# Kernel optimization log

Measured on AMD Instinct MI355X. Metric: run time of the kernel, lower is better.

Reference implementation:

```python
import jax, jax.numpy as jnp
import numpy as np

LORA_ALPHA = 2.0

def setup_inputs() -> dict:
    key = jax.random.key(0)
    k1, k2, k3, k4 = jax.random.split(key, 4)
    B, S, D_IN, D_OUT, R = 4, 2048, 4096, 4096, 16
    x = jax.random.normal(k1, (B, S, D_IN), dtype=jnp.float32)
    weight = jax.random.normal(k2, (D_OUT, D_IN), dtype=jnp.float32) * (1.0 / np.sqrt(D_IN))
    lora_A = jax.random.normal(k3, (R, D_IN), dtype=jnp.float32) * (1.0 / np.sqrt(D_IN))
    lora_B = jax.random.normal(k4, (D_OUT, R), dtype=jnp.float32) * 0.02
    return {"x": x, "weight": weight, "lora_A": lora_A, "lora_B": lora_B}

def reference(x, weight, lora_A, lora_B):
    # main_out = F.linear(x, weight) = x @ weight.T
    main_out = jnp.einsum('bsd,od->bso', x, weight)
    # Faithful to source: materialize lora_weight = B @ A (out x in), then full linear
    lora_weight = lora_B @ lora_A  # [out, in]
    lora_out = jnp.einsum('bsd,od->bso', x, lora_weight) * LORA_ALPHA
    return main_out + lora_out
```

## Files before the change

kernel.cpp:

```cpp
#include <hip/hip_runtime.h>
#include <stdint.h>

typedef __attribute__((ext_vector_type(8))) short bf16x8;
typedef __attribute__((ext_vector_type(4))) float f32x4;

#define GM 8192
#define GN 4096
#define GK 4096
#define KTILES (GK / 64)

__device__ __forceinline__ unsigned short f2bf(float f) {
  union { float f; unsigned int u; } c; c.f = f;
  unsigned int u = c.u;
  unsigned int r = u + 0x7FFFu + ((u >> 16) & 1u);
  return (unsigned short)(r >> 16);
}

__global__ __launch_bounds__(256) void cvt_x_kernel(const float* __restrict__ x,
                                                    unsigned short* __restrict__ xb) {
  int i = blockIdx.x * 256 + threadIdx.x;
  const float4* p = (const float4*)x + (size_t)i * 2;
  float4 a = p[0], b = p[1];
  unsigned short t[8] = { f2bf(a.x), f2bf(a.y), f2bf(a.z), f2bf(a.w),
                          f2bf(b.x), f2bf(b.y), f2bf(b.z), f2bf(b.w) };
  int4 pk; __builtin_memcpy(&pk, t, 16);
  ((int4*)xb)[i] = pk;
}

__global__ __launch_bounds__(256) void weff_kernel(const float* __restrict__ w,
                                                   const float* __restrict__ lA,
                                                   const float* __restrict__ lB,
                                                   unsigned short* __restrict__ wb) {
  const int K = GK;
  int idx = blockIdx.x * 256 + threadIdx.x;
  int cg = idx & 511;
  int rg = idx >> 9;
  int i0 = cg << 3;
  int o0 = rg << 3;

  float acc[8][8];
#pragma unroll
  for (int r = 0; r < 8; ++r)
#pragma unroll
    for (int c = 0; c < 8; ++c) acc[r][c] = 0.f;

#pragma unroll
  for (int r = 0; r < 16; ++r) {
    float4 a0 = *(const float4*)(lA + (size_t)r * K + i0);
    float4 a1 = *(const float4*)(lA + (size_t)r * K + i0 + 4);
    float av[8] = { a0.x, a0.y, a0.z, a0.w, a1.x, a1.y, a1.z, a1.w };
#pragma unroll
    for (int row = 0; row < 8; ++row) {
      float b = lB[(size_t)(o0 + row) * 16 + r];
#pragma unroll
      for (int c = 0; c < 8; ++c) acc[row][c] += b * av[c];
    }
  }

#pragma unroll
  for (int row = 0; row < 8; ++row) {
    float4 w0 = *(const float4*)(w + (size_t)(o0 + row) * K + i0);
    float4 w1 = *(const float4*)(w + (size_t)(o0 + row) * K + i0 + 4);
    unsigned short t[8] = {
      f2bf(w0.x + 2.0f * acc[row][0]), f2bf(w0.y + 2.0f * acc[row][1]),
      f2bf(w0.z + 2.0f * acc[row][2]), f2bf(w0.w + 2.0f * acc[row][3]),
      f2bf(w1.x + 2.0f * acc[row][4]), f2bf(w1.y + 2.0f * acc[row][5]),
      f2bf(w1.z + 2.0f * acc[row][6]), f2bf(w1.w + 2.0f * acc[row][7]) };
    int4 pk; __builtin_memcpy(&pk, t, 16);
    *(int4*)(wb + (size_t)(o0 + row) * K + i0) = pk;
  }
}


__device__ __forceinline__ void gload16(const unsigned short* g, char* l) {
  __builtin_amdgcn_global_load_lds((__attribute__((address_space(1))) void*)g,
                                   (__attribute__((address_space(3))) void*)l, 16, 0, 0);
}

__device__ __forceinline__ void bar() {
  asm volatile("" ::: "memory");
  __builtin_amdgcn_s_barrier();
  asm volatile("" ::: "memory");
}

#define MFMA_BF16(a, b, c) __builtin_amdgcn_mfma_f32_16x16x32_bf16((a), (b), (c), 0, 0, 0)

template <int HALF>
__device__ __forceinline__ void stage_half(const unsigned short* A, const unsigned short* B,
                                           char* smem, int bm0, int bn0, int w, int lane,
                                           int kt, int buf) {
  int sr, isB;
  if constexpr (HALF == 0)      { sr = w + (w & 4);                   isB = 0; }
  else if constexpr (HALF == 1) { sr = ((w >> 1) << 2) + (w & 1);     isB = 1; }
  else if constexpr (HALF == 2) { sr = ((w >> 1) << 2) + (w & 1) + 2; isB = 1; }
  else                          { sr = w + (w & 4) + 4;               isB = 0; }
  const unsigned short* mat = isB ? B : A;
  const int grow = (isB ? bn0 : bm0) + sr * 16 + (lane >> 2);
  const int gcol = ((lane & 3) * 8) ^ ((lane & 32) ? 16 : 0);
#pragma unroll
  for (int sc = 0; sc < 2; ++sc) {
    const unsigned short* src = mat + (size_t)grow * GK + kt * 64 + sc * 32 + gcol;
    char* dst = smem + (buf << 16) + (isB ? 32768 : 0) + ((sr * 2 + sc) << 10);
    gload16(src, dst);
  }
}

__device__ __forceinline__ bf16x8 ldsA(const char* smem, int buf, int sr, int sc, int foff) {
  return *(const bf16x8*)(smem + (buf << 16) + ((sr * 2 + sc) << 10) + foff);
}
__device__ __forceinline__ bf16x8 ldsB(const char* smem, int buf, int sr, int sc, int foff) {
  return *(const bf16x8*)(smem + (buf << 16) + 32768 + ((sr * 2 + sc) << 10) + foff);
}

__global__ __launch_bounds__(512, 2) void gemm_bt_kernel(const unsigned short* __restrict__ A,
                                                         const unsigned short* __restrict__ B,
                                                         float* __restrict__ C) {
  __shared__ alignas(16) char smem[131072];

  const int t = threadIdx.x, lane = t & 63, w = t >> 6;
  const int wm = w >> 2, wn = w & 3;

  const int bid = blockIdx.x;
  const int wg  = (bid & 7) * (512 / 8) + (bid >> 3);
  const int bx = wg & 15, by = wg >> 4;
  const int bm0 = by * 256, bn0 = bx * 256;

  int foff = (lane & 15) * 64 + ((lane >> 4) << 4);
  foff ^= ((foff >> 9) & 1) << 5;

  stage_half<0>(A, B, smem, bm0, bn0, w, lane, 0, 0);
  stage_half<1>(A, B, smem, bm0, bn0, w, lane, 0, 0);
  stage_half<2>(A, B, smem, bm0, bn0, w, lane, 0, 0);
  stage_half<3>(A, B, smem, bm0, bn0, w, lane, 0, 0);
  stage_half<0>(A, B, smem, bm0, bn0, w, lane, 1, 1);
  asm volatile("s_waitcnt vmcnt(6)" ::: "memory");
  bar();

  f32x4 acc[8][4] = {};
  bf16x8 av[4][2], bv0[2][2], bv1[2][2];

  for (int kt = 0; kt < KTILES; ++kt) {
    const int cur = kt & 1;
    const bool n1 = (kt + 1 < KTILES);
    const bool n2 = (kt + 2 < KTILES);

#pragma unroll
    for (int mi = 0; mi < 4; ++mi) {
      av[mi][0] = ldsA(smem, cur, wm * 8 + mi, 0, foff);
      av[mi][1] = ldsA(smem, cur, wm * 8 + mi, 1, foff);
    }
#pragma unroll
    for (int ni = 0; ni < 2; ++ni) {
      bv0[ni][0] = ldsB(smem, cur, wn * 4 + ni, 0, foff);
      bv0[ni][1] = ldsB(smem, cur, wn * 4 + ni, 1, foff);
    }
    if (n1) {
      stage_half<1>(A, B, smem, bm0, bn0, w, lane, kt + 1, cur ^ 1);
      asm volatile("s_waitcnt vmcnt(6)" ::: "memory");
    } else {
      asm volatile("s_waitcnt vmcnt(2)" ::: "memory");
    }
    bar();
    asm volatile("s_waitcnt lgkmcnt(0)" ::: "memory");
    __builtin_amdgcn_s_setprio(1);
#pragma unroll
    for (int mi = 0; mi < 4; ++mi)
#pragma unroll
      for (int ni = 0; ni < 2; ++ni) {
        acc[mi][ni] = MFMA_BF16(av[mi][0], bv0[ni][0], acc[mi][ni]);
        acc[mi][ni] = MFMA_BF16(av[mi][1], bv0[ni][1], acc[mi][ni]);
      }
    __builtin_amdgcn_s_setprio(0);
    bar();

#pragma unroll
    for (int ni = 0; ni < 2; ++ni) {
      bv1[ni][0] = ldsB(smem, cur, wn * 4 + 2 + ni, 0, foff);
      bv1[ni][1] = ldsB(smem, cur, wn * 4 + 2 + ni, 1, foff);
    }
    if (n1) {
      stage_half<2>(A, B, smem, bm0, bn0, w, lane, kt + 1, cur ^ 1);
      asm volatile("s_waitcnt vmcnt(6)" ::: "memory");
    } else {
      asm volatile("s_waitcnt vmcnt(0)" ::: "memory");
    }
    bar();
    asm volatile("s_waitcnt lgkmcnt(0)" ::: "memory");
    __builtin_amdgcn_s_setprio(1);
#pragma unroll
    for (int mi = 0; mi < 4; ++mi)
#pragma unroll
      for (int ni = 0; ni < 2; ++ni) {
        acc[mi][2 + ni] = MFMA_BF16(av[mi][0], bv1[ni][0], acc[mi][2 + ni]);
        acc[mi][2 + ni] = MFMA_BF16(av[mi][1], bv1[ni][1], acc[mi][2 + ni]);
      }
    __builtin_amdgcn_s_setprio(0);
    bar();

#pragma unroll
    for (int mi = 0; mi < 4; ++mi) {
      av[mi][0] = ldsA(smem, cur, wm * 8 + 4 + mi, 0, foff);
      av[mi][1] = ldsA(smem, cur, wm * 8 + 4 + mi, 1, foff);
    }
    if (n1) stage_half<3>(A, B, smem, bm0, bn0, w, lane, kt + 1, cur ^ 1);
    bar();
    asm volatile("s_waitcnt lgkmcnt(0)" ::: "memory");
    __builtin_amdgcn_s_setprio(1);
#pragma unroll
    for (int mi = 0; mi < 4; ++mi)
#pragma unroll
      for (int ni = 0; ni < 2; ++ni) {
        acc[4 + mi][2 + ni] = MFMA_BF16(av[mi][0], bv1[ni][0], acc[4 + mi][2 + ni]);
        acc[4 + mi][2 + ni] = MFMA_BF16(av[mi][1], bv1[ni][1], acc[4 + mi][2 + ni]);
      }
    __builtin_amdgcn_s_setprio(0);
    bar();

    if (n2) stage_half<0>(A, B, smem, bm0, bn0, w, lane, kt + 2, cur);
    if (n1) {
      if (n2) asm volatile("s_waitcnt vmcnt(6)" ::: "memory");
      else    asm volatile("s_waitcnt vmcnt(4)" ::: "memory");
    }
    bar();
    __builtin_amdgcn_s_setprio(1);
#pragma unroll
    for (int mi = 0; mi < 4; ++mi)
#pragma unroll
      for (int ni = 0; ni < 2; ++ni) {
        acc[4 + mi][ni] = MFMA_BF16(av[mi][0], bv0[ni][0], acc[4 + mi][ni]);
        acc[4 + mi][ni] = MFMA_BF16(av[mi][1], bv0[ni][1], acc[4 + mi][ni]);
      }
    __builtin_amdgcn_s_setprio(0);
    bar();
  }

  const int orow = (lane >> 4) << 2;
#pragma unroll
  for (int mi = 0; mi < 8; ++mi) {
#pragma unroll
    for (int ni = 0; ni < 4; ++ni) {
      float* cp = C + (size_t)(bm0 + wm * 128 + mi * 16 + orow) * GN
                    + (bn0 + wn * 64 + ni * 16 + (lane & 15));
#pragma unroll
      for (int r = 0; r < 4; ++r)
        cp[(size_t)r * GN] = acc[mi][ni][r];
    }
  }
}

extern "C" void kernel_launch(void* const* d_in, const int* in_sizes, int n_in,
                              void* d_out, int out_size, void* d_ws, size_t ws_size,
                              hipStream_t stream) {
  const float* x  = (const float*)d_in[0];
  const float* w  = (const float*)d_in[1];
  const float* lA = (const float*)d_in[2];
  const float* lB = (const float*)d_in[3];
  float* out = (float*)d_out;

  const int M = GM, N = GN, K = GK;

  unsigned short* xb = (unsigned short*)d_ws;
  unsigned short* wb = xb + (size_t)M * K;

  cvt_x_kernel<<<dim3((M * K / 8) / 256), dim3(256), 0, stream>>>(x, xb);
  weff_kernel<<<dim3((N / 8) * (K / 8) / 256), dim3(256), 0, stream>>>(w, lA, lB, wb);
  gemm_bt_kernel<<<dim3((M / 256) * (N / 256)), dim3(512), 0, stream>>>(xb, wb, out);
}
```

Measured before the change: 293.5 us.

## Interleave LDS fragment loads with MFMA and drop per-phase barriers

Restructures the GEMM main loop so each LDS fragment read is issued during the preceding MFMA block instead of before it. Fragments for the next k-tile are prefetched at the end of the current iteration, and the phase-end barriers plus explicit lgkmcnt waits are removed so fewer syncs sit on the critical path. The intent is to hide LDS read latency behind matrix math. The risk is LDS hazards between buffer reuse and global-to-LDS staging once barriers are gone, and higher register pressure.

```diff
diff --git a/kernel.cpp b/kernel.cpp
--- a/kernel.cpp
+++ b/kernel.cpp
@@ -139,99 +139,101 @@
   f32x4 acc[8][4] = {};
   bf16x8 av[4][2], bv0[2][2], bv1[2][2];
 
+#pragma unroll
+  for (int mi = 0; mi < 4; ++mi) {
+    av[mi][0] = ldsA(smem, 0, wm * 8 + mi, 0, foff);
+    av[mi][1] = ldsA(smem, 0, wm * 8 + mi, 1, foff);
+  }
+#pragma unroll
+  for (int ni = 0; ni < 2; ++ni) {
+    bv0[ni][0] = ldsB(smem, 0, wn * 4 + ni, 0, foff);
+    bv0[ni][1] = ldsB(smem, 0, wn * 4 + ni, 1, foff);
+  }
+
   for (int kt = 0; kt < KTILES; ++kt) {
-    const int cur = kt & 1;
+    const int cur = kt & 1, nxt = cur ^ 1;
     const bool n1 = (kt + 1 < KTILES);
     const bool n2 = (kt + 2 < KTILES);
 
-#pragma unroll
-    for (int mi = 0; mi < 4; ++mi) {
-      av[mi][0] = ldsA(smem, cur, wm * 8 + mi, 0, foff);
-      av[mi][1] = ldsA(smem, cur, wm * 8 + mi, 1, foff);
-    }
-#pragma unroll
-    for (int ni = 0; ni < 2; ++ni) {
-      bv0[ni][0] = ldsB(smem, cur, wn * 4 + ni, 0, foff);
-      bv0[ni][1] = ldsB(smem, cur, wn * 4 + ni, 1, foff);
-    }
     if (n1) {
-      stage_half<1>(A, B, smem, bm0, bn0, w, lane, kt + 1, cur ^ 1);
+      stage_half<1>(A, B, smem, bm0, bn0, w, lane, kt + 1, nxt);
       asm volatile("s_waitcnt vmcnt(6)" ::: "memory");
     } else {
       asm volatile("s_waitcnt vmcnt(2)" ::: "memory");
     }
     bar();
-    asm volatile("s_waitcnt lgkmcnt(0)" ::: "memory");
-    __builtin_amdgcn_s_setprio(1);
-#pragma unroll
-    for (int mi = 0; mi < 4; ++mi)
-#pragma unroll
-      for (int ni = 0; ni < 2; ++ni) {
-        acc[mi][ni] = MFMA_BF16(av[mi][0], bv0[ni][0], acc[mi][ni]);
-        acc[mi][ni] = MFMA_BF16(av[mi][1], bv0[ni][1], acc[mi][ni]);
-      }
-    __builtin_amdgcn_s_setprio(0);
-    bar();
-
 #pragma unroll
     for (int ni = 0; ni < 2; ++ni) {
       bv1[ni][0] = ldsB(smem, cur, wn * 4 + 2 + ni, 0, foff);
       bv1[ni][1] = ldsB(smem, cur, wn * 4 + 2 + ni, 1, foff);
     }
+    __builtin_amdgcn_sched_barrier(0);
+    __builtin_amdgcn_s_setprio(1);
+#pragma unroll
+    for (int mi = 0; mi < 4; ++mi) {
+      acc[mi][0] = MFMA_BF16(av[mi][0], bv0[0][0], acc[mi][0]);
+      acc[mi][0] = MFMA_BF16(av[mi][1], bv0[0][1], acc[mi][0]);
+      acc[mi][1] = MFMA_BF16(av[mi][0], bv0[1][0], acc[mi][1]);
+      acc[mi][1] = MFMA_BF16(av[mi][1], bv0[1][1], acc[mi][1]);
+    }
+    __builtin_amdgcn_s_setprio(0);
+
     if (n1) {
-      stage_half<2>(A, B, smem, bm0, bn0, w, lane, kt + 1, cur ^ 1);
+      stage_half<2>(A, B, smem, bm0, bn0, w, lane, kt + 1, nxt);
       asm volatile("s_waitcnt vmcnt(6)" ::: "memory");
     } else {
       asm volatile("s_waitcnt vmcnt(0)" ::: "memory");
     }
     bar();
-    asm volatile("s_waitcnt lgkmcnt(0)" ::: "memory");
-    __builtin_amdgcn_s_setprio(1);
-#pragma unroll
-    for (int mi = 0; mi < 4; ++mi)
-#pragma unroll
-      for (int ni = 0; ni < 2; ++ni) {
-        acc[mi][2 + ni] = MFMA_BF16(av[mi][0], bv1[ni][0], acc[mi][2 + ni]);
-        acc[mi][2 + ni] = MFMA_BF16(av[mi][1], bv1[ni][1], acc[mi][2 + ni]);
-      }
-    __builtin_amdgcn_s_setprio(0);
-    bar();
-
+    __builtin_amdgcn_s_setprio(1);
 #pragma unroll
     for (int mi = 0; mi < 4; ++mi) {
+      acc[mi][2] = MFMA_BF16(av[mi][0], bv1[0][0], acc[mi][2]);
+      acc[mi][2] = MFMA_BF16(av[mi][1], bv1[0][1], acc[mi][2]);
+      acc[mi][3] = MFMA_BF16(av[mi][0], bv1[1][0], acc[mi][3]);
+      acc[mi][3] = MFMA_BF16(av[mi][1], bv1[1][1], acc[mi][3]);
       av[mi][0] = ldsA(smem, cur, wm * 8 + 4 + mi, 0, foff);
       av[mi][1] = ldsA(smem, cur, wm * 8 + 4 + mi, 1, foff);
     }
-    if (n1) stage_half<3>(A, B, smem, bm0, bn0, w, lane, kt + 1, cur ^ 1);
-    bar();
-    asm volatile("s_waitcnt lgkmcnt(0)" ::: "memory");
-    __builtin_amdgcn_s_setprio(1);
-#pragma unroll
-    for (int mi = 0; mi < 4; ++mi)
-#pragma unroll
-      for (int ni = 0; ni < 2; ++ni) {
-        acc[4 + mi][2 + ni] = MFMA_BF16(av[mi][0], bv1[ni][0], acc[4 + mi][2 + ni]);
-        acc[4 + mi][2 + ni] = MFMA_BF16(av[mi][1], bv1[ni][1], acc[4 + mi][2 + ni]);
-      }
-    __builtin_amdgcn_s_setprio(0);
-    bar();
+    __builtin_amdgcn_s_setprio(0);
+
+    if (n1) stage_half<3>(A, B, smem, bm0, bn0, w, lane, kt + 1, nxt);
+    bar();
+    __builtin_amdgcn_s_setprio(1);
+#pragma unroll
+    for (int mi = 0; mi < 4; ++mi) {
+      acc[4 + mi][2] = MFMA_BF16(av[mi][0], bv1[0][0], acc[4 + mi][2]);
+      acc[4 + mi][2] = MFMA_BF16(av[mi][1], bv1[0][1], acc[4 + mi][2]);
+      acc[4 + mi][3] = MFMA_BF16(av[mi][0], bv1[1][0], acc[4 + mi][3]);
+      acc[4 + mi][3] = MFMA_BF16(av[mi][1], bv1[1][1], acc[4 + mi][3]);
+    }
+    __builtin_amdgcn_s_setprio(0);
 
     if (n2) stage_half<0>(A, B, smem, bm0, bn0, w, lane, kt + 2, cur);
-    if (n1) {
-      if (n2) asm volatile("s_waitcnt vmcnt(6)" ::: "memory");
-      else    asm volatile("s_waitcnt vmcnt(4)" ::: "memory");
-    }
-    bar();
-    __builtin_amdgcn_s_setprio(1);
-#pragma unroll
-    for (int mi = 0; mi < 4; ++mi)
-#pragma unroll
-      for (int ni = 0; ni < 2; ++ni) {
+    if (n2)      { asm volatile("s_waitcnt vmcnt(6)" ::: "memory"); }
+    else if (n1) { asm volatile("s_waitcnt vmcnt(4)" ::: "memory"); }
+    bar();
+    __builtin_amdgcn_s_setprio(1);
+#pragma unroll
+    for (int ni = 0; ni < 2; ++ni) {
+#pragma unroll
+      for (int mi = 0; mi < 4; ++mi) {
         acc[4 + mi][ni] = MFMA_BF16(av[mi][0], bv0[ni][0], acc[4 + mi][ni]);
         acc[4 + mi][ni] = MFMA_BF16(av[mi][1], bv0[ni][1], acc[4 + mi][ni]);
       }
-    __builtin_amdgcn_s_setprio(0);
-    bar();
+      if (n1) {
+        bv0[ni][0] = ldsB(smem, nxt, wn * 4 + ni, 0, foff);
+        bv0[ni][1] = ldsB(smem, nxt, wn * 4 + ni, 1, foff);
+      }
+    }
+    if (n1) {
+#pragma unroll
+      for (int mi = 0; mi < 4; ++mi) {
+        av[mi][0] = ldsA(smem, nxt, wm * 8 + mi, 0, foff);
+        av[mi][1] = ldsA(smem, nxt, wm * 8 + mi, 1, foff);
+      }
+    }
+    __builtin_amdgcn_s_setprio(0);
   }
 
   const int orow = (lane >> 4) << 2;
```

Measured after the change: 288.1 us. No clear change (-1.8%).
